# Optimization experiments

Measured on AMD Instinct MI355X. Metric: run time of the kernel, lower is better.

## Reference

```python
import math
import jax, jax.numpy as jnp
import numpy as np

B, S, D, H, FF = 2, 2048, 1024, 16, 4096
HD = D // H  # head dim = 64
EPS = 1e-12


def setup_inputs() -> dict:
    key = jax.random.key(0)
    ks = jax.random.split(key, 16)
    w = lambda k, shape: (jax.random.normal(k, shape, jnp.float32) * 0.02)
    return {
        "hidden_states": jax.random.normal(ks[0], (B, S, D), jnp.float32),
        "attention_mask": jnp.zeros((B, 1, 1, S), jnp.float32),
        "wq": w(ks[1], (D, D)), "bq": jnp.zeros((D,), jnp.float32),
        "wk": w(ks[2], (D, D)), "bk": jnp.zeros((D,), jnp.float32),
        "wv": w(ks[3], (D, D)), "bv": jnp.zeros((D,), jnp.float32),
        "wo": w(ks[4], (D, D)), "bo": jnp.zeros((D,), jnp.float32),
        "w1": w(ks[5], (D, FF)), "b1": jnp.zeros((FF,), jnp.float32),
        "w2": w(ks[6], (FF, D)), "b2": jnp.zeros((D,), jnp.float32),
        "g1": jnp.ones((D,), jnp.float32), "be1": jnp.zeros((D,), jnp.float32),
        "g2": jnp.ones((D,), jnp.float32), "be2": jnp.zeros((D,), jnp.float32),
    }


def _layernorm(x, g, b):
    mu = jnp.mean(x, axis=-1, keepdims=True)
    var = jnp.mean(jnp.square(x - mu), axis=-1, keepdims=True)
    return (x - mu) * jax.lax.rsqrt(var + EPS) * g + b


def _gelu_erf(x):
    # x * 0.5 * (1 + erf(x / sqrt(2)))  -- exact erf gelu as in source
    return x * 0.5 * (1.0 + jax.lax.erf(x / math.sqrt(2.0)))


def _attention(x, mask, wq, bq, wk, bk, wv, bv, wo, bo):
    b, s, d = x.shape
    split = lambda t: t.reshape(b, s, H, HD).transpose(0, 2, 1, 3)  # [b,h,s,hd]
    q = split(x @ wq + bq)
    k = split(x @ wk + bk)
    v = split(x @ wv + bv)
    scores = jnp.einsum("bhqd,bhkd->bhqk", q, k) / math.sqrt(HD)
    scores = scores + mask  # broadcast [b,1,1,s]
    probs = jax.nn.softmax(scores, axis=-1)
    ctx = jnp.einsum("bhqk,bhkd->bhqd", probs, v)
    ctx = ctx.transpose(0, 2, 1, 3).reshape(b, s, d)
    return ctx @ wo + bo


def reference(hidden_states, attention_mask, wq, bq, wk, bk, wv, bv, wo, bo,
              w1, b1, w2, b2, g1, be1, g2, be2):
    # prenorm transformer layer (dropout = identity in eval)
    residual = hidden_states
    h = _layernorm(hidden_states, g1, be1)
    attn = _attention(h, attention_mask, wq, bq, wk, bk, wv, bv, wo, bo)
    h = residual + attn
    residual = h
    h2 = _layernorm(h, g2, be2)
    ff = _gelu_erf(h2 @ w1 + b1) @ w2 + b2
    return residual + ff
```

## Files before the change

kernel.cpp:

```cpp
#include <hip/hip_runtime.h>
#include <hip/hip_bf16.h>
#include <math.h>


#define BB 2
#define SS 2048
#define DD 1024
#define HH 16
#define HDIM 64
#define FFD 4096
#define NTOK (BB*SS)
#define LOG2E 1.4426950408889634f

typedef __attribute__((ext_vector_type(8))) short bf16x8;
typedef __attribute__((ext_vector_type(4))) float f32x4;
typedef __attribute__((ext_vector_type(16))) float f32x16;
typedef __attribute__((ext_vector_type(4))) unsigned int u32x4;

#if __has_builtin(__builtin_amdgcn_exp2f)
#define EXP2(x) __builtin_amdgcn_exp2f(x)
#else
#define EXP2(x) exp2f(x)
#endif

__device__ __forceinline__ void gl_lds16(const void* g, void* l) {
  __builtin_amdgcn_global_load_lds(
      (const __attribute__((address_space(1))) unsigned int*)g,
      (__attribute__((address_space(3))) unsigned int*)l, 16, 0, 0);
}

__device__ __forceinline__ short f2bf(float f) {
  unsigned int u = __builtin_bit_cast(unsigned int, f);
  unsigned int r = (u + 0x7fffu + ((u >> 16) & 1u)) >> 16;
  return (short)r;
}
__device__ __forceinline__ unsigned pk2(float lo, float hi) {
  return (unsigned)(unsigned short)f2bf(lo) | ((unsigned)(unsigned short)f2bf(hi) << 16);
}

__global__ __launch_bounds__(256) void convT(const float* __restrict__ w,
                                             __hip_bfloat16* __restrict__ wt,
                                             int K, int N) {
  __shared__ float tile[32][33];
  int k0 = blockIdx.y * 32, n0 = blockIdx.x * 32;
  int tx = threadIdx.x & 31, ty = threadIdx.x >> 5;
#pragma unroll
  for (int i = 0; i < 4; ++i) {
    int r = ty + i * 8;
    tile[r][tx] = w[(size_t)(k0 + r) * N + n0 + tx];
  }
  __syncthreads();
#pragma unroll
  for (int i = 0; i < 4; ++i) {
    int r = ty + i * 8;
    wt[(size_t)(n0 + r) * K + k0 + tx] = __float2bfloat16(tile[tx][r]);
  }
}

__global__ __launch_bounds__(256) void ln_bf16(const float* __restrict__ x,
                                               const float* __restrict__ g,
                                               const float* __restrict__ be,
                                               __hip_bfloat16* __restrict__ out) {
  int w = threadIdx.x >> 6, lane = threadIdx.x & 63;
  int row = blockIdx.x * 4 + w;
  const float* xr = x + (size_t)row * DD;
  float4 v[4];
  float sum = 0.f, sq = 0.f;
#pragma unroll
  for (int i = 0; i < 4; ++i) {
    v[i] = *(const float4*)(xr + lane * 4 + i * 256);
    sum += v[i].x + v[i].y + v[i].z + v[i].w;
    sq += v[i].x * v[i].x + v[i].y * v[i].y + v[i].z * v[i].z + v[i].w * v[i].w;
  }
#pragma unroll
  for (int off = 1; off < 64; off <<= 1) {
    sum += __shfl_xor(sum, off);
    sq += __shfl_xor(sq, off);
  }
  float mu = sum * (1.f / 1024.f);
  float var = sq * (1.f / 1024.f) - mu * mu;
  float rs = rsqrtf(var + 1e-12f);
  __hip_bfloat16* orow = out + (size_t)row * DD;
#pragma unroll
  for (int i = 0; i < 4; ++i) {
    int c = lane * 4 + i * 256;
    float4 gg = *(const float4*)(g + c);
    float4 bb = *(const float4*)(be + c);
    short4 o;
    o.x = f2bf((v[i].x - mu) * rs * gg.x + bb.x);
    o.y = f2bf((v[i].y - mu) * rs * gg.y + bb.y);
    o.z = f2bf((v[i].z - mu) * rs * gg.z + bb.z);
    o.w = f2bf((v[i].w - mu) * rs * gg.w + bb.w);
    *(short4*)((short*)orow + c) = o;
  }
}

template <int EPI>
__global__ __launch_bounds__(256, 4) void gemm_bt(
    const __hip_bfloat16* __restrict__ A, const __hip_bfloat16* __restrict__ BT,
    const float* __restrict__ bA, const float* __restrict__ bB,
    const float* __restrict__ bC,
    void* __restrict__ C0, void* __restrict__ C1, void* __restrict__ C2,
    int M, int N, int K, int kSplit) {
  __shared__ __align__(16) char smem[34816];
  short* As = (short*)smem;
  short* Bs = (short*)(smem + 8192);
  const int t = threadIdx.x, lane = t & 63, w = t >> 6;
  const int m0 = blockIdx.y * 128, n0 = blockIdx.x * 128;
  const int wm = (w >> 1) * 64, wn = (w & 1) * 64;
  const int row16 = lane & 15, grp = lane >> 4;
  const int arow = t >> 2, achunk = t & 3;
  f32x4 acc[4][4] = {};

  const int steps = K >> 5;
  const int z = blockIdx.z;
  const int sBeg = (z * steps) / kSplit, sEnd = ((z + 1) * steps) / kSplit;

  for (int s = sBeg; s < sEnd; ++s) {
    const int kt = s << 5;
    __syncthreads();
#pragma unroll
    for (int j = 0; j < 2; ++j) {
      int r = arow + j * 64;
      gl_lds16(A + (size_t)(m0 + r) * K + kt + achunk * 8,
               (char*)As + r * 64 + achunk * 16);
      gl_lds16(BT + (size_t)(n0 + r) * K + kt + achunk * 8,
               (char*)Bs + r * 64 + achunk * 16);
    }
    __syncthreads();
    bf16x8 af[4], bfr[4];
#pragma unroll
    for (int f = 0; f < 4; ++f) {
      af[f] = *(const bf16x8*)((const char*)As + (wm + f * 16 + row16) * 64 + grp * 16);
      bfr[f] = *(const bf16x8*)((const char*)Bs + (wn + f * 16 + row16) * 64 + grp * 16);
    }
#pragma unroll
    for (int mf = 0; mf < 4; ++mf)
#pragma unroll
      for (int nf = 0; nf < 4; ++nf)
        acc[mf][nf] =
            __builtin_amdgcn_mfma_f32_16x16x32_bf16(af[mf], bfr[nf], acc[mf][nf], 0, 0, 0);
  }

  __syncthreads();

  if constexpr (EPI == 5) {
    if (n0 >= 2048) {
#pragma unroll
      for (int nf = 0; nf < 4; ++nf) {
        int vloc = wn + nf * 16 + row16;
        float bv = bC[n0 - 2048 + vloc];
#pragma unroll
        for (int mf = 0; mf < 4; ++mf) {
          int tloc = wm + mf * 16 + grp * 4;
          f32x4 a = acc[mf][nf];
          *(uint2*)(smem + vloc * 272 + tloc * 2) =
              make_uint2(pk2(a[0] + bv, a[1] + bv), pk2(a[2] + bv, a[3] + bv));
        }
      }
      __syncthreads();
      int vrBase = ((m0 >> 11) << 10) + (n0 - 2048);
      int mcol = m0 & 2047;
#pragma unroll
      for (int i = 0; i < 8; ++i) {
        int c = t + i * 256;
        int vr = c >> 4, tc = c & 15;
        u32x4 vv = *(const u32x4*)(smem + vr * 272 + tc * 16);
        *(u32x4*)((__hip_bfloat16*)C2 + (size_t)(vrBase + vr) * 2048 + mcol + tc * 8) = vv;
      }
      return;
    }
  }

  __hip_bfloat16* outP = nullptr;
  int ldO = N, colB = n0;
  const float* bp = nullptr;
  if constexpr (EPI == 1) { outP = (__hip_bfloat16*)C0; bp = bA; }
  if constexpr (EPI == 5) {
    const bool isK = n0 >= 1024;
    outP = (__hip_bfloat16*)(isK ? C1 : C0);
    bp = isK ? bB : bA;
    ldO = 1024; colB = n0 & 1023;
  }
  if constexpr (EPI == 7) outP = (__hip_bfloat16*)C0 + (size_t)z * 4194304ull;
  if constexpr (EPI == 8)
    outP = (__hip_bfloat16*)C0 + ((z == 0) ? 0ull : ((z == 1) ? 4194304ull : 12582912ull));

#pragma unroll
  for (int nf = 0; nf < 4; ++nf) {
    int nn = wn + nf * 16 + row16;
    float bv = bp ? bp[colB + nn] : 0.f;
#pragma unroll
    for (int mf = 0; mf < 4; ++mf) {
      int mloc = wm + mf * 16 + grp * 4;
      f32x4 a = acc[mf][nf];
#pragma unroll
      for (int r = 0; r < 4; ++r) {
        float v = a[r] + bv;
        if constexpr (EPI == 1)
          v = 0.5f * v * (1.0f + erff(v * 0.70710678118654752f));
        *(short*)(smem + (mloc + r) * 272 + nn * 2) = f2bf(v);
      }
    }
  }
  __syncthreads();
#pragma unroll
  for (int i = 0; i < 8; ++i) {
    int c = t + i * 256;
    int mmr = c >> 4, nc = c & 15;
    u32x4 vv = *(const u32x4*)(smem + mmr * 272 + nc * 16);
    *(u32x4*)(outP + (size_t)(m0 + mmr) * ldO + colB + nc * 8) = vv;
  }
}

__global__ __launch_bounds__(256) void reduce3(const __hip_bfloat16* __restrict__ p0,
                                               const __hip_bfloat16* __restrict__ p1,
                                               const __hip_bfloat16* __restrict__ p2,
                                               const float* __restrict__ h1,
                                               const float* __restrict__ b2,
                                               float* __restrict__ out) {
  int idx = (blockIdx.x * 256 + threadIdx.x) * 8;
  int n = idx & 1023;
  bf16x8 a = *(const bf16x8*)(p0 + idx);
  bf16x8 b = *(const bf16x8*)(p1 + idx);
  bf16x8 c = *(const bf16x8*)(p2 + idx);
  float4 hA = *(const float4*)(h1 + idx), hB = *(const float4*)(h1 + idx + 4);
  float4 bA = *(const float4*)(b2 + n), bB = *(const float4*)(b2 + n + 4);
  float o[8];
#pragma unroll
  for (int j = 0; j < 8; ++j) {
    float fa = __builtin_bit_cast(float, ((unsigned)(unsigned short)a[j]) << 16);
    float fb = __builtin_bit_cast(float, ((unsigned)(unsigned short)b[j]) << 16);
    float fc = __builtin_bit_cast(float, ((unsigned)(unsigned short)c[j]) << 16);
    o[j] = fa + fb + fc;
  }
  float4 r0 = make_float4(o[0] + hA.x + bA.x, o[1] + hA.y + bA.y,
                          o[2] + hA.z + bA.z, o[3] + hA.w + bA.w);
  float4 r1 = make_float4(o[4] + hB.x + bB.x, o[5] + hB.y + bB.y,
                          o[6] + hB.z + bB.z, o[7] + hB.w + bB.w);
  *(float4*)(out + idx) = r0;
  *(float4*)(out + idx + 4) = r1;
}

__global__ __launch_bounds__(256) void reduce4(const __hip_bfloat16* __restrict__ p0,
                                               const __hip_bfloat16* __restrict__ p1,
                                               const __hip_bfloat16* __restrict__ p2,
                                               const __hip_bfloat16* __restrict__ p3,
                                               const float* __restrict__ x,
                                               const float* __restrict__ bo,
                                               float* __restrict__ out) {
  int idx = (blockIdx.x * 256 + threadIdx.x) * 8;
  int n = idx & 1023;
  bf16x8 a = *(const bf16x8*)(p0 + idx);
  bf16x8 b = *(const bf16x8*)(p1 + idx);
  bf16x8 c = *(const bf16x8*)(p2 + idx);
  bf16x8 d = *(const bf16x8*)(p3 + idx);
  float4 hA = *(const float4*)(x + idx), hB = *(const float4*)(x + idx + 4);
  float4 bA = *(const float4*)(bo + n), bB = *(const float4*)(bo + n + 4);
  float o[8];
#pragma unroll
  for (int j = 0; j < 8; ++j) {
    float fa = __builtin_bit_cast(float, ((unsigned)(unsigned short)a[j]) << 16);
    float fb = __builtin_bit_cast(float, ((unsigned)(unsigned short)b[j]) << 16);
    float fc = __builtin_bit_cast(float, ((unsigned)(unsigned short)c[j]) << 16);
    float fd = __builtin_bit_cast(float, ((unsigned)(unsigned short)d[j]) << 16);
    o[j] = (fa + fb) + (fc + fd);
  }
  float4 r0 = make_float4(o[0] + hA.x + bA.x, o[1] + hA.y + bA.y,
                          o[2] + hA.z + bA.z, o[3] + hA.w + bA.w);
  float4 r1 = make_float4(o[4] + hB.x + bB.x, o[5] + hB.y + bB.y,
                          o[6] + hB.z + bB.z, o[7] + hB.w + bB.w);
  *(float4*)(out + idx) = r0;
  *(float4*)(out + idx + 4) = r1;
}

__global__ __launch_bounds__(512) void flash_attn2(
    const __hip_bfloat16* __restrict__ Q,
    const __hip_bfloat16* __restrict__ Kg,
    const __hip_bfloat16* __restrict__ VTg,
    const float* __restrict__ mask,
    __hip_bfloat16* __restrict__ O) {
  __shared__ __align__(16) char lds[33280];
  const int t = threadIdx.x, lane = t & 63, w = t >> 6;
  const int l31 = lane & 31, hi = lane >> 5;
  const int q0 = blockIdx.x * 256;
  const int bh = blockIdx.y, b = bh >> 4, h = bh & 15;
  const int qrow = q0 + w * 32 + l31;

  bf16x8 qf[4];
  {
    const __hip_bfloat16* qp = Q + ((size_t)(b * SS + qrow)) * DD + h * HDIM + hi * 8;
    qf[0] = *(const bf16x8*)(qp);
    qf[1] = *(const bf16x8*)(qp + 16);
    qf[2] = *(const bf16x8*)(qp + 32);
    qf[3] = *(const bf16x8*)(qp + 48);
  }
  f32x16 ctx0 = {}, ctx1 = {};
  float m = -1e30f, l = 0.f, mC = -1.44e30f;

  auto stage = [&](int buf, int kv0) {
    int r = t >> 3, c = t & 7;
    gl_lds16(Kg + ((size_t)(b * SS + kv0 + r)) * DD + h * HDIM + ((c ^ (r & 7)) * 8),
             lds + buf * 8192 + t * 16);
    gl_lds16(VTg + ((size_t)(bh * 64 + r)) * 2048 + kv0 + ((c ^ (r & 7)) * 8),
             lds + 16384 + buf * 8192 + t * 16);
    if (t < 64) *(float*)(lds + 32768 + buf * 256 + t * 4) = mask[b * SS + kv0 + t];
  };

  stage(0, 0);
  for (int it = 0; it < SS / 64; ++it) {
    __syncthreads();
    if (it + 1 < SS / 64) stage((it + 1) & 1, (it + 1) * 64);
    const char* Kb = lds + (it & 1) * 8192;
    const char* Vb = lds + 16384 + (it & 1) * 8192;
    const float* mk = (const float*)(lds + 32768 + (it & 1) * 256);

    f32x16 s0 = {}, s1 = {};
#pragma unroll
    for (int kc = 0; kc < 4; ++kc) {
      int c = kc * 2 + hi;
      int r0 = l31, r1 = 32 + l31;
      bf16x8 ka0 = *(const bf16x8*)(Kb + r0 * 128 + ((c ^ (r0 & 7)) << 4));
      bf16x8 ka1 = *(const bf16x8*)(Kb + r1 * 128 + ((c ^ (r1 & 7)) << 4));
      s0 = __builtin_amdgcn_mfma_f32_32x32x16_bf16(ka0, qf[kc], s0, 0, 0, 0);
      s1 = __builtin_amdgcn_mfma_f32_32x32x16_bf16(ka1, qf[kc], s1, 0, 0, 0);
    }
#pragma unroll
    for (int g = 0; g < 4; ++g) {
      float4 mg0 = *(const float4*)(mk + g * 8 + hi * 4);
      float4 mg1 = *(const float4*)(mk + 32 + g * 8 + hi * 4);
      const float* m0p = (const float*)&mg0;
      const float* m1p = (const float*)&mg1;
#pragma unroll
      for (int i = 0; i < 4; ++i) {
        s0[g * 4 + i] = fmaf(s0[g * 4 + i], 0.125f, m0p[i]);
        s1[g * 4 + i] = fmaf(s1[g * 4 + i], 0.125f, m1p[i]);
      }
    }
    float pmax;
    {
      f32x16 q8;
#pragma unroll
      for (int r = 0; r < 16; ++r) q8[r] = fmaxf(s0[r], s1[r]);
#pragma unroll
      for (int r = 0; r < 8; ++r) q8[r] = fmaxf(q8[r], q8[r + 8]);
#pragma unroll
      for (int r = 0; r < 4; ++r) q8[r] = fmaxf(q8[r], q8[r + 4]);
      pmax = fmaxf(fmaxf(q8[0], q8[1]), fmaxf(q8[2], q8[3]));
      pmax = fmaxf(pmax, __shfl_xor(pmax, 32));
    }
    if (__any(pmax > m + 8.0f)) {
      float mnew = fmaxf(m, pmax);
      float fac = EXP2((m - mnew) * LOG2E);
      l *= fac;
#pragma unroll
      for (int r = 0; r < 16; ++r) { ctx0[r] *= fac; ctx1[r] *= fac; }
      m = mnew;
      mC = m * LOG2E;
    }
    float rsA = 0.f, rsB = 0.f;
#pragma unroll
    for (int r = 0; r < 16; ++r) {
      s0[r] = EXP2(fmaf(s0[r], LOG2E, -mC));
      s1[r] = EXP2(fmaf(s1[r], LOG2E, -mC));
      rsA += s0[r];
      rsB += s1[r];
    }
    rsA += rsB;
    rsA += __shfl_xor(rsA, 32);
    l += rsA;

    unsigned W0[8], W1[8];
#pragma unroll
    for (int g = 0; g < 4; ++g) {
      W0[g * 2] = pk2(s0[g * 4 + 0], s0[g * 4 + 1]);
      W0[g * 2 + 1] = pk2(s0[g * 4 + 2], s0[g * 4 + 3]);
      W1[g * 2] = pk2(s1[g * 4 + 0], s1[g * 4 + 1]);
      W1[g * 2 + 1] = pk2(s1[g * 4 + 2], s1[g * 4 + 3]);
    }
    unsigned swA0 = __shfl_xor(hi ? W0[0] : W0[2], 32);
    unsigned swA1 = __shfl_xor(hi ? W0[1] : W0[3], 32);
    unsigned swB0 = __shfl_xor(hi ? W0[4] : W0[6], 32);
    unsigned swB1 = __shfl_xor(hi ? W0[5] : W0[7], 32);
    unsigned swC0 = __shfl_xor(hi ? W1[0] : W1[2], 32);
    unsigned swC1 = __shfl_xor(hi ? W1[1] : W1[3], 32);
    unsigned swD0 = __shfl_xor(hi ? W1[4] : W1[6], 32);
    unsigned swD1 = __shfl_xor(hi ? W1[5] : W1[7], 32);
    u32x4 pb[4];
    pb[0] = hi ? (u32x4){swA0, swA1, W0[2], W0[3]} : (u32x4){W0[0], W0[1], swA0, swA1};
    pb[1] = hi ? (u32x4){swB0, swB1, W0[6], W0[7]} : (u32x4){W0[4], W0[5], swB0, swB1};
    pb[2] = hi ? (u32x4){swC0, swC1, W1[2], W1[3]} : (u32x4){W1[0], W1[1], swC0, swC1};
    pb[3] = hi ? (u32x4){swD0, swD1, W1[6], W1[7]} : (u32x4){W1[4], W1[5], swD0, swD1};

#pragma unroll
    for (int kc = 0; kc < 4; ++kc) {
      bf16x8 pbf = __builtin_bit_cast(bf16x8, pb[kc]);
      int c = kc * 2 + hi;
      int r0 = l31, r1 = 32 + l31;
      bf16x8 va0 = *(const bf16x8*)(Vb + r0 * 128 + ((c ^ (r0 & 7)) << 4));
      bf16x8 va1 = *(const bf16x8*)(Vb + r1 * 128 + ((c ^ (r1 & 7)) << 4));
      ctx0 = __builtin_amdgcn_mfma_f32_32x32x16_bf16(va0, pbf, ctx0, 0, 0, 0);
      ctx1 = __builtin_amdgcn_mfma_f32_32x32x16_bf16(va1, pbf, ctx1, 0, 0, 0);
    }
  }

  float inv = 1.0f / l;
#pragma unroll
  for (int r = 0; r < 16; ++r) { ctx0[r] *= inv; ctx1[r] *= inv; }
  __syncthreads();
  {
    int row = w * 32 + l31;
#pragma unroll
    for (int dt = 0; dt < 2; ++dt) {
#pragma unroll
      for (int g = 0; g < 4; ++g) {
        unsigned lo2 = dt ? pk2(ctx1[g * 4 + 0], ctx1[g * 4 + 1]) : pk2(ctx0[g * 4 + 0], ctx0[g * 4 + 1]);
        unsigned hi2 = dt ? pk2(ctx1[g * 4 + 2], ctx1[g * 4 + 3]) : pk2(ctx0[g * 4 + 2], ctx0[g * 4 + 3]);
        int c = dt * 4 + g;
        *(uint2*)(lds + row * 128 + ((c ^ (row & 7)) << 4) + hi * 8) = make_uint2(lo2, hi2);
      }
    }
  }
  __syncthreads();
  {
    int r = t >> 1;
    size_t tok = (size_t)(b * SS + q0 + r);
#pragma unroll
    for (int i = 0; i < 4; ++i) {
      int c = (t & 1) * 4 + i;
      u32x4 vv = *(const u32x4*)(lds + r * 128 + ((c ^ (r & 7)) << 4));
      *(u32x4*)((short*)O + tok * DD + h * HDIM + c * 8) = vv;
    }
  }
}

extern "C" void kernel_launch(void* const* d_in, const int* in_sizes, int n_in,
                              void* d_out, int out_size, void* d_ws, size_t ws_size,
                              hipStream_t stream) {
  const float* x = (const float*)d_in[0];
  const float* mask = (const float*)d_in[1];
  const float* wq = (const float*)d_in[2];
  const float* bq = (const float*)d_in[3];
  const float* wk = (const float*)d_in[4];
  const float* bk = (const float*)d_in[5];
  const float* wv = (const float*)d_in[6];
  const float* bv = (const float*)d_in[7];
  const float* wo = (const float*)d_in[8];
  const float* bo = (const float*)d_in[9];
  const float* w1 = (const float*)d_in[10];
  const float* b1 = (const float*)d_in[11];
  const float* w2 = (const float*)d_in[12];
  const float* b2 = (const float*)d_in[13];
  const float* g1 = (const float*)d_in[14];
  const float* be1 = (const float*)d_in[15];
  const float* g2 = (const float*)d_in[16];
  const float* be2 = (const float*)d_in[17];

  char* ws = (char*)d_ws;
  const size_t MB = 1024ull * 1024ull;
  __hip_bfloat16* wqkvT = (__hip_bfloat16*)(ws + 0 * MB);
  __hip_bfloat16* woT = (__hip_bfloat16*)(ws + 6 * MB);
  __hip_bfloat16* w1T = (__hip_bfloat16*)(ws + 8 * MB);
  __hip_bfloat16* w2T = (__hip_bfloat16*)(ws + 16 * MB);
  __hip_bfloat16* xn = (__hip_bfloat16*)(ws + 24 * MB);
  __hip_bfloat16* qb = (__hip_bfloat16*)(ws + 32 * MB);
  __hip_bfloat16* kb = (__hip_bfloat16*)(ws + 40 * MB);
  __hip_bfloat16* vtb = (__hip_bfloat16*)(ws + 48 * MB);
  __hip_bfloat16* ctxb = (__hip_bfloat16*)(ws + 56 * MB);
  float* h1 = (float*)(ws + 64 * MB);
  __hip_bfloat16* h2 = xn;
  __hip_bfloat16* a1 = qb;

  convT<<<dim3(32, 32), 256, 0, stream>>>(wq, wqkvT, 1024, 1024);
  convT<<<dim3(32, 32), 256, 0, stream>>>(wk, wqkvT + 1024 * 1024, 1024, 1024);
  convT<<<dim3(32, 32), 256, 0, stream>>>(wv, wqkvT + 2 * 1024 * 1024, 1024, 1024);
  convT<<<dim3(32, 32), 256, 0, stream>>>(wo, woT, 1024, 1024);
  convT<<<dim3(128, 32), 256, 0, stream>>>(w1, w1T, 1024, 4096);
  convT<<<dim3(32, 128), 256, 0, stream>>>(w2, w2T, 4096, 1024);

  ln_bf16<<<1024, 256, 0, stream>>>(x, g1, be1, xn);

  gemm_bt<5><<<dim3(24, 32), 256, 0, stream>>>(
      xn, wqkvT, bq, bk, bv, qb, kb, vtb, NTOK, 3072, 1024, 1);

  flash_attn2<<<dim3(8, 32), 512, 0, stream>>>(qb, kb, vtb, mask, ctxb);

  gemm_bt<7><<<dim3(8, 32, 4), 256, 0, stream>>>(
      ctxb, woT, nullptr, nullptr, nullptr, ws + 24 * MB, nullptr, nullptr,
      NTOK, 1024, 1024, 4);

  reduce4<<<2048, 256, 0, stream>>>((__hip_bfloat16*)(ws + 24 * MB),
                                    (__hip_bfloat16*)(ws + 32 * MB),
                                    (__hip_bfloat16*)(ws + 40 * MB),
                                    (__hip_bfloat16*)(ws + 48 * MB),
                                    x, bo, h1);

  ln_bf16<<<1024, 256, 0, stream>>>(h1, g2, be2, h2);

  gemm_bt<1><<<dim3(32, 32), 256, 0, stream>>>(
      h2, w1T, b1, nullptr, nullptr, a1, nullptr, nullptr, NTOK, FFD, 1024, 1);

  gemm_bt<8><<<dim3(8, 32, 3), 256, 0, stream>>>(
      a1, w2T, nullptr, nullptr, nullptr, ws, nullptr, nullptr,
      NTOK, 1024, FFD, 3);

  reduce3<<<2048, 256, 0, stream>>>((__hip_bfloat16*)(ws + 0 * MB),
                                    (__hip_bfloat16*)(ws + 8 * MB),
                                    (__hip_bfloat16*)(ws + 24 * MB),
                                    h1, b2, (float*)d_out);
}
```

Measured before the change: 284.9 us.

## Split flash attention over two KV halves and merge partials

The attention kernel now splits the KV sequence in two along a new grid z dimension. Each half writes unnormalized bf16 partial contexts plus per-row max and sum, and a new merge kernel combines them with log-sum-exp weights. The original grid of 256 blocks of 512 threads likely underfilled the GPU, so this doubles parallelism at the cost of an extra kernel launch and extra global traffic. It also replaces the manual bf16 pack with the v_cvt_pk_bf16_f32 instruction. Storing unnormalized partials in bf16 adds a small precision risk.

```diff
diff --git a/kernel.cpp b/kernel.cpp
--- a/kernel.cpp
+++ b/kernel.cpp
@@ -34,8 +34,13 @@
   unsigned int r = (u + 0x7fffu + ((u >> 16) & 1u)) >> 16;
   return (short)r;
 }
+__device__ __forceinline__ float bf2f(short s) {
+  return __builtin_bit_cast(float, ((unsigned)(unsigned short)s) << 16);
+}
 __device__ __forceinline__ unsigned pk2(float lo, float hi) {
-  return (unsigned)(unsigned short)f2bf(lo) | ((unsigned)(unsigned short)f2bf(hi) << 16);
+  unsigned r;
+  asm("v_cvt_pk_bf16_f32 %0, %1, %2" : "=v"(r) : "v"(lo), "v"(hi));
+  return r;
 }
 
 __global__ __launch_bounds__(256) void convT(const float* __restrict__ w,
@@ -228,12 +233,7 @@
   float4 bA = *(const float4*)(b2 + n), bB = *(const float4*)(b2 + n + 4);
   float o[8];
 #pragma unroll
-  for (int j = 0; j < 8; ++j) {
-    float fa = __builtin_bit_cast(float, ((unsigned)(unsigned short)a[j]) << 16);
-    float fb = __builtin_bit_cast(float, ((unsigned)(unsigned short)b[j]) << 16);
-    float fc = __builtin_bit_cast(float, ((unsigned)(unsigned short)c[j]) << 16);
-    o[j] = fa + fb + fc;
-  }
+  for (int j = 0; j < 8; ++j) o[j] = bf2f(a[j]) + bf2f(b[j]) + bf2f(c[j]);
   float4 r0 = make_float4(o[0] + hA.x + bA.x, o[1] + hA.y + bA.y,
                           o[2] + hA.z + bA.z, o[3] + hA.w + bA.w);
   float4 r1 = make_float4(o[4] + hB.x + bB.x, o[5] + hB.y + bB.y,
@@ -259,13 +259,8 @@
   float4 bA = *(const float4*)(bo + n), bB = *(const float4*)(bo + n + 4);
   float o[8];
 #pragma unroll
-  for (int j = 0; j < 8; ++j) {
-    float fa = __builtin_bit_cast(float, ((unsigned)(unsigned short)a[j]) << 16);
-    float fb = __builtin_bit_cast(float, ((unsigned)(unsigned short)b[j]) << 16);
-    float fc = __builtin_bit_cast(float, ((unsigned)(unsigned short)c[j]) << 16);
-    float fd = __builtin_bit_cast(float, ((unsigned)(unsigned short)d[j]) << 16);
-    o[j] = (fa + fb) + (fc + fd);
-  }
+  for (int j = 0; j < 8; ++j)
+    o[j] = (bf2f(a[j]) + bf2f(b[j])) + (bf2f(c[j]) + bf2f(d[j]));
   float4 r0 = make_float4(o[0] + hA.x + bA.x, o[1] + hA.y + bA.y,
                           o[2] + hA.z + bA.z, o[3] + hA.w + bA.w);
   float4 r1 = make_float4(o[4] + hB.x + bB.x, o[5] + hB.y + bB.y,
@@ -279,12 +274,17 @@
     const __hip_bfloat16* __restrict__ Kg,
     const __hip_bfloat16* __restrict__ VTg,
     const float* __restrict__ mask,
-    __hip_bfloat16* __restrict__ O) {
+    __hip_bfloat16* __restrict__ pctx0,
+    __hip_bfloat16* __restrict__ pctx1,
+    float2* __restrict__ ml) {
   __shared__ __align__(16) char lds[33280];
   const int t = threadIdx.x, lane = t & 63, w = t >> 6;
   const int l31 = lane & 31, hi = lane >> 5;
   const int q0 = blockIdx.x * 256;
   const int bh = blockIdx.y, b = bh >> 4, h = bh & 15;
+  const int z = blockIdx.z;
+  const int kvBase = z * (SS / 2);
+  __hip_bfloat16* pctx = z ? pctx1 : pctx0;
   const int qrow = q0 + w * 32 + l31;
 
   bf16x8 qf[4];
@@ -307,10 +307,11 @@
     if (t < 64) *(float*)(lds + 32768 + buf * 256 + t * 4) = mask[b * SS + kv0 + t];
   };
 
-  stage(0, 0);
-  for (int it = 0; it < SS / 64; ++it) {
+  stage(0, kvBase);
+  const int NIT = SS / 128;
+  for (int it = 0; it < NIT; ++it) {
     __syncthreads();
-    if (it + 1 < SS / 64) stage((it + 1) & 1, (it + 1) * 64);
+    if (it + 1 < NIT) stage((it + 1) & 1, kvBase + (it + 1) * 64);
     const char* Kb = lds + (it & 1) * 8192;
     const char* Vb = lds + 16384 + (it & 1) * 8192;
     const float* mk = (const float*)(lds + 32768 + (it & 1) * 256);
@@ -404,9 +405,8 @@
     }
   }
 
-  float inv = 1.0f / l;
-#pragma unroll
-  for (int r = 0; r < 16; ++r) { ctx0[r] *= inv; ctx1[r] *= inv; }
+  if (hi == 0) ml[((size_t)z * NTOK + b * SS + qrow) * HH + h] = make_float2(m, l);
+
   __syncthreads();
   {
     int row = w * 32 + l31;
@@ -429,9 +429,30 @@
     for (int i = 0; i < 4; ++i) {
       int c = (t & 1) * 4 + i;
       u32x4 vv = *(const u32x4*)(lds + r * 128 + ((c ^ (r & 7)) << 4));
-      *(u32x4*)((short*)O + tok * DD + h * HDIM + c * 8) = vv;
-    }
-  }
+      *(u32x4*)((short*)pctx + tok * DD + h * HDIM + c * 8) = vv;
+    }
+  }
+}
+
+__global__ __launch_bounds__(256) void mergeAttn(
+    const __hip_bfloat16* __restrict__ p0, const __hip_bfloat16* __restrict__ p1,
+    const float2* __restrict__ ml, __hip_bfloat16* __restrict__ out) {
+  int tok = blockIdx.x, tid = threadIdx.x;
+  int h = tid >> 4;
+  float2 a = ml[(size_t)tok * HH + h];
+  float2 b = ml[(size_t)(NTOK + tok) * HH + h];
+  float M = fmaxf(a.x, b.x);
+  float w0 = EXP2((a.x - M) * LOG2E), w1 = EXP2((b.x - M) * LOG2E);
+  float inv = 1.0f / (w0 * a.y + w1 * b.y);
+  w0 *= inv; w1 *= inv;
+  size_t idx = (size_t)tok * DD + tid * 4;
+  short4 c0 = *(const short4*)((const short*)p0 + idx);
+  short4 c1 = *(const short4*)((const short*)p1 + idx);
+  unsigned lo = pk2(w0 * bf2f(c0.x) + w1 * bf2f(c1.x),
+                    w0 * bf2f(c0.y) + w1 * bf2f(c1.y));
+  unsigned hi2 = pk2(w0 * bf2f(c0.z) + w1 * bf2f(c1.z),
+                     w0 * bf2f(c0.w) + w1 * bf2f(c1.w));
+  *(uint2*)((short*)out + idx) = make_uint2(lo, hi2);
 }
 
 extern "C" void kernel_launch(void* const* d_in, const int* in_sizes, int n_in,
@@ -470,6 +491,9 @@
   float* h1 = (float*)(ws + 64 * MB);
   __hip_bfloat16* h2 = xn;
   __hip_bfloat16* a1 = qb;
+  __hip_bfloat16* pctx0 = (__hip_bfloat16*)(ws + 24 * MB);
+  __hip_bfloat16* pctx1 = (__hip_bfloat16*)(ws + 64 * MB);
+  float2* mlbuf = (float2*)(ws + 72 * MB);
 
   convT<<<dim3(32, 32), 256, 0, stream>>>(wq, wqkvT, 1024, 1024);
   convT<<<dim3(32, 32), 256, 0, stream>>>(wk, wqkvT + 1024 * 1024, 1024, 1024);
@@ -483,7 +507,9 @@
   gemm_bt<5><<<dim3(24, 32), 256, 0, stream>>>(
       xn, wqkvT, bq, bk, bv, qb, kb, vtb, NTOK, 3072, 1024, 1);
 
-  flash_attn2<<<dim3(8, 32), 512, 0, stream>>>(qb, kb, vtb, mask, ctxb);
+  flash_attn2<<<dim3(8, 32, 2), 512, 0, stream>>>(qb, kb, vtb, mask,
+                                                  pctx0, pctx1, mlbuf);
+  mergeAttn<<<4096, 256, 0, stream>>>(pctx0, pctx1, mlbuf, ctxb);
 
   gemm_bt<7><<<dim3(8, 32, 4), 256, 0, stream>>>(
       ctxb, woT, nullptr, nullptr, nullptr, ws + 24 * MB, nullptr, nullptr,
```

Result: no change. 287.9 us (+1.1%).
